# Optimization experiments

Hardware: AMD Instinct MI355X
Metric: run time of the kernel (lower is better)

Reference implementation:

```python
import jax, jax.numpy as jnp
import numpy as np

N = 100000   # nodes
E = 3200000  # edges
D = 256      # hidden_dim
G = 512      # graphs in batch
NEG_SLOPE = 0.2


def segment_softmax(logits, seg, num_segments):
    # numerically stable per-segment softmax over dim 0
    m = jax.ops.segment_max(logits, seg, num_segments=num_segments)
    m = jnp.where(jnp.isfinite(m), m, 0.0)  # empty segments -> 0
    e = jnp.exp(logits - m[seg])
    s = jax.ops.segment_sum(e, seg, num_segments=num_segments)
    return e / (s[seg] + 1e-16)


def setup_inputs() -> dict:
    key = jax.random.key(0)
    ks = jax.random.split(key, 6)
    x = jax.random.normal(ks[0], (N, D), dtype=jnp.float32)
    edge_index = jax.random.randint(ks[1], (2, E), 0, N, dtype=jnp.int32)
    batch = jnp.sort(jax.random.randint(ks[2], (N,), 0, G, dtype=jnp.int32))
    # GATConv(hidden_dim, 1) params (heads=1): lin weight, att vectors, bias
    W = jax.random.normal(ks[3], (D, 1), dtype=jnp.float32) / np.sqrt(D).astype(np.float32)
    att_src = jax.random.normal(ks[4], (1,), dtype=jnp.float32)
    att_dst = jax.random.normal(ks[5], (1,), dtype=jnp.float32)
    bias = jnp.zeros((1,), dtype=jnp.float32)
    return {"x": x, "edge_index": edge_index, "batch": batch,
            "W": W, "att_src": att_src, "att_dst": att_dst, "bias": bias}


def reference(x, edge_index, batch, W, att_src, att_dst, bias):
    n = x.shape[0]
    # --- GATConv(hidden_dim, 1), heads=1, add_self_loops=True ---
    h = x @ W                               # [N,1]
    a_s = (h * att_src).squeeze(-1)         # [N]
    a_d = (h * att_dst).squeeze(-1)         # [N]
    loops = jnp.arange(n, dtype=edge_index.dtype)
    src = jnp.concatenate([edge_index[0], loops])   # [E+N]
    dst = jnp.concatenate([edge_index[1], loops])   # [E+N]
    e = jax.nn.leaky_relu(a_s[src] + a_d[dst], NEG_SLOPE)
    alpha = segment_softmax(e, dst, n)               # softmax over incoming edges
    x_conv = jax.ops.segment_sum(alpha[:, None] * h[src], dst, num_segments=n) + bias  # [N,1]
    # --- segment softmax over graphs, then scatter-add pooling ---
    scores = segment_softmax(x_conv.squeeze(-1), batch, G)[:, None]  # [N,1]
    gx = jax.ops.segment_sum(x * scores, batch, num_segments=G)       # [G,D]
    return gx
```

## Files before the change

### kernel.cpp

```cpp
#include <hip/hip_runtime.h>
#include <stdint.h>

#define NEG_SLOPE 0.2f
#define DHID 256
#define BSZ_SHIFT 10
#define BSZ (1 << BSZ_SHIFT)
#define MAXNB 128
#define PSUB 16
#define SCHUNK 4096
#define KSUB 4

__device__ __forceinline__ float lrelu(float e) {
    return (e >= 0.0f) ? e : NEG_SLOPE * e;
}
__device__ __forceinline__ float dot4(float4 a, float4 b) {
    return a.x * b.x + a.y * b.y + a.z * b.z + a.w * b.w;
}

__global__ __launch_bounds__(256) void k1_h_bounds(
    const float* __restrict__ x, const float* __restrict__ W,
    float* __restrict__ h, int N,
    const int* __restrict__ batch, int* __restrict__ start, int G,
    float* __restrict__ gsum, int* __restrict__ cursor, int NB,
    int nRowBlk, int nBndBlk)
{
    if (blockIdx.x >= (unsigned)nRowBlk) {
        int rb = blockIdx.x - nRowBlk;
        if (rb == nBndBlk) {
            for (int t = threadIdx.x; t < G; t += 256) gsum[t] = 0.0f;
            for (int t = threadIdx.x; t < NB; t += 256) cursor[t] = 0;
            return;
        }
        int i = rb * 256 + threadIdx.x;
        if (i >= N) return;
        int b = batch[i];
        if (i == 0) {
            for (int g = 0; g <= b; ++g) start[g] = 0;
        } else {
            int bp = batch[i - 1];
            for (int g = bp + 1; g <= b; ++g) start[g] = i;
        }
        if (i == N - 1) {
            for (int g = b + 1; g <= G; ++g) start[g] = N;
        }
        return;
    }

    int wave = threadIdx.x >> 6;
    int lane = threadIdx.x & 63;
    int r = lane >> 4;
    int c = lane & 15;
    int row = blockIdx.x * 16 + wave * 4 + r;
    if (row >= N) return;

    float4 wv0 = *(const float4*)(W + c * 4);
    float4 wv1 = *(const float4*)(W + 64 + c * 4);
    float4 wv2 = *(const float4*)(W + 128 + c * 4);
    float4 wv3 = *(const float4*)(W + 192 + c * 4);
    const float* xr = x + (size_t)row * DHID;
    float4 a0 = *(const float4*)(xr + c * 4);
    float4 a1 = *(const float4*)(xr + 64 + c * 4);
    float4 a2 = *(const float4*)(xr + 128 + c * 4);
    float4 a3 = *(const float4*)(xr + 192 + c * 4);
    float s = dot4(a0, wv0) + dot4(a1, wv1) + dot4(a2, wv2) + dot4(a3, wv3);
    s += __shfl_xor(s, 1);
    s += __shfl_xor(s, 2);
    s += __shfl_xor(s, 4);
    s += __shfl_xor(s, 8);
    if (c == 0) h[row] = s;
}

__global__ __launch_bounds__(512) void k_scatter(
    const int* __restrict__ src, const int* __restrict__ dst, int E, int NB,
    int* __restrict__ cursor, uint32_t* __restrict__ pairs, int CAP)
{
    __shared__ int cnt[MAXNB];
    __shared__ int loff[MAXNB];
    __shared__ int base_g[MAXNB];
    __shared__ int lcur[MAXNB];
    __shared__ uint32_t buf[SCHUNK];
    __shared__ uint8_t binOf[SCHUNK];

    int e0 = blockIdx.x * SCHUNK;
    int e1 = min(e0 + SCHUNK, E);
    int nch = e1 - e0;
    int t = threadIdx.x;

    int sv[8], dv[8];
#pragma unroll
    for (int k = 0; k < 8; ++k) {
        int e = e0 + k * 512 + t;
        if (e < e1) { sv[k] = src[e]; dv[k] = dst[e]; }
    }

    for (int q = t; q < MAXNB; q += 512) { cnt[q] = 0; lcur[q] = 0; }
    __syncthreads();
#pragma unroll
    for (int k = 0; k < 8; ++k) {
        int e = e0 + k * 512 + t;
        if (e < e1) atomicAdd(&cnt[dv[k] >> BSZ_SHIFT], 1);
    }
    __syncthreads();
    if (t < 64) {
        int v0 = cnt[t], v1 = cnt[64 + t];
        int s0 = v0, s1 = v1;
#pragma unroll
        for (int d = 1; d < 64; d <<= 1) {
            int u0 = __shfl_up(s0, d);
            int u1 = __shfl_up(s1, d);
            if (t >= d) { s0 += u0; s1 += u1; }
        }
        int tot0 = __shfl(s0, 63);
        loff[t]      = s0 - v0;
        loff[64 + t] = s1 + tot0 - v1;
    }
    __syncthreads();
    for (int q = t; q < MAXNB; q += 512)
        if (q < NB && cnt[q] > 0) base_g[q] = atomicAdd(&cursor[q], cnt[q]);
    __syncthreads();
#pragma unroll
    for (int k = 0; k < 8; ++k) {
        int e = e0 + k * 512 + t;
        if (e < e1) {
            int d = dv[k];
            int bin = d >> BSZ_SHIFT;
            int r = atomicAdd(&lcur[bin], 1);
            int q = loff[bin] + r;
            buf[q] = ((uint32_t)sv[k] << BSZ_SHIFT) | (uint32_t)(d & (BSZ - 1));
            binOf[q] = (uint8_t)bin;
        }
    }
    __syncthreads();
    for (int q = t; q < nch; q += 512) {
        int b = binOf[q];
        pairs[(size_t)b * CAP + base_g[b] + (q - loff[b])] = buf[q];
    }
}

__global__ __launch_bounds__(256) void k_accum(
    const uint32_t* __restrict__ pairs, const int* __restrict__ cursor,
    const float* __restrict__ h,
    const float* __restrict__ att_src, const float* __restrict__ att_dst,
    float* __restrict__ partials, int N, int CAP)
{
    __shared__ float dacc[BSZ];
    __shared__ float nacc[BSZ];
    __shared__ float hbuf[BSZ];
    int b = blockIdx.x / PSUB;
    int s = blockIdx.x % PSUB;
    int base = b << BSZ_SHIFT;

    for (int t = threadIdx.x; t < BSZ; t += 256) {
        dacc[t] = 0.0f; nacc[t] = 0.0f;
        int gi = base + t;
        hbuf[t] = (gi < N) ? h[gi] : 0.0f;
    }
    __syncthreads();

    int count = cursor[b];
    int per = (count + PSUB - 1) / PSUB;
    int i0 = s * per;
    int i1 = min(i0 + per, count);

    float as = att_src[0], ad = att_dst[0];
    const uint32_t* bp = pairs + (size_t)b * CAP;
    for (int i = i0 + threadIdx.x; i < i1; i += 256) {
        uint32_t pr = bp[i];
        int ld = (int)(pr & (BSZ - 1));
        float hs = h[pr >> BSZ_SHIFT];
        float w = __expf(lrelu(as * hs + ad * hbuf[ld]));
        atomicAdd(&dacc[ld], w);
        atomicAdd(&nacc[ld], w * hs);
    }
    __syncthreads();
    float* out = partials + ((size_t)blockIdx.x * 2) * BSZ;
    for (int t = threadIdx.x; t < BSZ; t += 256) {
        out[t]       = dacc[t];
        out[BSZ + t] = nacc[t];
    }
}

__global__ __launch_bounds__(256) void k3_scores_p(
    const float* __restrict__ partials, const float* __restrict__ h,
    const float* __restrict__ att_src, const float* __restrict__ att_dst,
    const float* __restrict__ bias, const int* __restrict__ batch,
    float* __restrict__ escore, float* __restrict__ gsum, int N)
{
    __shared__ float bins[64];
    __shared__ int bbase_s;
    int i = blockIdx.x * 256 + threadIdx.x;
    if (threadIdx.x == 0) {
        int i0 = blockIdx.x * 256;
        bbase_s = batch[i0 < N ? i0 : N - 1];
    }
    for (int t = threadIdx.x; t < 64; t += 256) bins[t] = 0.0f;

    float w = 0.0f;
    int b = -1;
    if (i < N) {
        int bk = i >> BSZ_SHIFT;
        int pos = i & (BSZ - 1);
        float dsum = 0.0f, nsum = 0.0f;
#pragma unroll
        for (int p = 0; p < PSUB; ++p) {
            const float* pp = partials + ((size_t)(bk * PSUB + p) * 2) * BSZ;
            dsum += pp[pos];
            nsum += pp[BSZ + pos];
        }
        float hi = h[i];
        float e0 = lrelu((att_src[0] + att_dst[0]) * hi);
        float ws = __expf(e0);
        dsum += ws;
        nsum += ws * hi;
        float xc = nsum / (dsum + 1e-16f) + bias[0];
        w = __expf(xc);
        escore[i] = w;
        b = batch[i];
    }
    __syncthreads();
    if (i < N) {
        int off = b - bbase_s;
        if (off >= 0 && off < 64) atomicAdd(&bins[off], w);
        else                      atomicAdd(&gsum[b], w);
    }
    __syncthreads();
    for (int t = threadIdx.x; t < 64; t += 256)
        if (bins[t] != 0.0f) atomicAdd(&gsum[bbase_s + t], bins[t]);
}

__global__ __launch_bounds__(256) void k4_pool(
    const float* __restrict__ x, const float* __restrict__ escore,
    const float* __restrict__ gsum, const int* __restrict__ start,
    float* __restrict__ gxp, int G)
{
    int g = blockIdx.x >> 2;
    int s = blockIdx.x & 3;
    int st = start[g], en = start[g + 1];
    float inv = 1.0f / (gsum[g] + 1e-16f);
    int tid    = threadIdx.x;
    int col4   = (tid & 63) << 2;
    int rowOff = tid >> 6;

    float4 acc = make_float4(0.f, 0.f, 0.f, 0.f);
    int i = st + s * 4 + rowOff;
    for (; i + 16 < en; i += 32) {
        float sc0 = escore[i] * inv;
        float sc1 = escore[i + 16] * inv;
        float4 v0 = *(const float4*)(x + (size_t)i * DHID + col4);
        float4 v1 = *(const float4*)(x + (size_t)(i + 16) * DHID + col4);
        acc.x += v0.x * sc0 + v1.x * sc1;
        acc.y += v0.y * sc0 + v1.y * sc1;
        acc.z += v0.z * sc0 + v1.z * sc1;
        acc.w += v0.w * sc0 + v1.w * sc1;
    }
    if (i < en) {
        float sc = escore[i] * inv;
        float4 v = *(const float4*)(x + (size_t)i * DHID + col4);
        acc.x += v.x * sc; acc.y += v.y * sc;
        acc.z += v.z * sc; acc.w += v.w * sc;
    }

    __shared__ float4 red[256];
    red[tid] = acc;
    __syncthreads();
    if (tid < 64) {
        float4 a = red[tid], b = red[tid + 64], c = red[tid + 128], d = red[tid + 192];
        float4 r;
        r.x = a.x + b.x + c.x + d.x;
        r.y = a.y + b.y + c.y + d.y;
        r.z = a.z + b.z + c.z + d.z;
        r.w = a.w + b.w + c.w + d.w;
        *(float4*)(gxp + ((size_t)s * G + g) * DHID + col4) = r;
    }
}

__global__ __launch_bounds__(256) void k5_merge(
    const float* __restrict__ gxp, float* __restrict__ gx, int total)
{
    int j = blockIdx.x * 256 + threadIdx.x;
    if (j < total)
        gx[j] = gxp[j] + gxp[total + j] + gxp[2 * total + j] + gxp[3 * total + j];
}

__global__ __launch_bounds__(256) void k0_zero_fb(float* __restrict__ p, int n) {
    int i = blockIdx.x * 256 + threadIdx.x;
    if (i < n) p[i] = 0.0f;
}
__global__ __launch_bounds__(256) void k2_edges_fb(
    const int* __restrict__ src, const int* __restrict__ dst,
    const float* __restrict__ h,
    const float* __restrict__ att_src, const float* __restrict__ att_dst,
    float* __restrict__ denom, float* __restrict__ num, int E)
{
    int i = blockIdx.x * 256 + threadIdx.x;
    if (i >= E) return;
    int s = src[i], d = dst[i];
    float as = att_src[0], ad = att_dst[0];
    float hs = h[s];
    float w = expf(lrelu(as * hs + ad * h[d]));
    atomicAdd(&denom[d], w);
    atomicAdd(&num[d],   w * hs);
}
__global__ __launch_bounds__(256) void k3_scores_fb(
    const float* __restrict__ denom, const float* __restrict__ num,
    const float* __restrict__ h,
    const float* __restrict__ att_src, const float* __restrict__ att_dst,
    const float* __restrict__ bias, const int* __restrict__ batch,
    float* __restrict__ escore, float* __restrict__ gsum, int N)
{
    __shared__ float bins[64];
    __shared__ int bbase_s;
    int i = blockIdx.x * 256 + threadIdx.x;
    if (threadIdx.x == 0) {
        int i0 = blockIdx.x * 256;
        bbase_s = batch[i0 < N ? i0 : N - 1];
    }
    for (int t = threadIdx.x; t < 64; t += 256) bins[t] = 0.0f;
    float w = 0.0f;
    int b = -1;
    if (i < N) {
        float hi = h[i];
        float ws = expf(lrelu((att_src[0] + att_dst[0]) * hi));
        float dsum = denom[i] + ws;
        float nsum = num[i] + ws * hi;
        float xc = nsum / (dsum + 1e-16f) + bias[0];
        w = expf(xc);
        escore[i] = w;
        b = batch[i];
    }
    __syncthreads();
    if (i < N) {
        int off = b - bbase_s;
        if (off >= 0 && off < 64) atomicAdd(&bins[off], w);
        else                      atomicAdd(&gsum[b], w);
    }
    __syncthreads();
    for (int t = threadIdx.x; t < 64; t += 256)
        if (bins[t] != 0.0f) atomicAdd(&gsum[bbase_s + t], bins[t]);
}

extern "C" void kernel_launch(void* const* d_in, const int* in_sizes, int n_in,
                              void* d_out, int out_size, void* d_ws, size_t ws_size,
                              hipStream_t stream) {
    const float* x        = (const float*)d_in[0];
    const int*   eidx     = (const int*)d_in[1];
    const int*   batch    = (const int*)d_in[2];
    const float* W        = (const float*)d_in[3];
    const float* att_src  = (const float*)d_in[4];
    const float* att_dst  = (const float*)d_in[5];
    const float* bias     = (const float*)d_in[6];
    float*       gx       = (float*)d_out;

    const int N = in_sizes[2];
    const int E = in_sizes[1] / 2;
    const int G = out_size / DHID;
    const int NB = (N + BSZ - 1) >> BSZ_SHIFT;
    const int CAP = ((E / NB + 8192) + 255) & ~255;

    const int* src = eidx;
    const int* dst = eidx + E;

    char* p = (char*)d_ws;
    auto alloc = [&](size_t bytes) {
        char* q = p;
        p += (bytes + 255) & ~(size_t)255;
        return q;
    };
    float* h      = (float*)alloc((size_t)N * 4);
    float* escore = (float*)alloc((size_t)N * 4);
    float* gsum   = (float*)alloc((size_t)G * 4);
    int*   startA = (int*)alloc((size_t)(G + 1) * 4);

    size_t fixed = (size_t)(p - (char*)d_ws);
    size_t need_full = fixed
        + 512 + (size_t)NB * 4
        + 512 + (size_t)NB * CAP * 4
        + 512 + (size_t)NB * PSUB * 2 * BSZ * 4
        + 512 + (size_t)KSUB * G * DHID * 4;

    bool full = (NB <= MAXNB) && (N <= (1 << (32 - BSZ_SHIFT)))
             && (need_full + 4096 <= ws_size);

    int nRowBlk = (N + 15) / 16;
    int nBndBlk = (N + 255) / 256;

    if (full) {
        int*      cursor   = (int*)alloc((size_t)NB * 4);
        uint32_t* pairs    = (uint32_t*)alloc((size_t)NB * CAP * 4);
        float*    partials = (float*)alloc((size_t)NB * PSUB * 2 * BSZ * 4);
        float*    gxp      = (float*)alloc((size_t)KSUB * G * DHID * 4);

        int sgrid = (E + SCHUNK - 1) / SCHUNK;

        k1_h_bounds<<<nRowBlk + nBndBlk + 1, 256, 0, stream>>>(
            x, W, h, N, batch, startA, G, gsum, cursor, NB, nRowBlk, nBndBlk);
        k_scatter<<<sgrid, 512, 0, stream>>>(src, dst, E, NB, cursor,
                                             pairs, CAP);
        k_accum<<<NB * PSUB, 256, 0, stream>>>(pairs, cursor, h,
                                               att_src, att_dst, partials,
                                               N, CAP);
        k3_scores_p<<<(N + 255) / 256, 256, 0, stream>>>(partials, h,
                                                         att_src, att_dst, bias,
                                                         batch, escore, gsum, N);
        k4_pool<<<G * KSUB, 256, 0, stream>>>(x, escore, gsum, startA, gxp, G);
        k5_merge<<<(G * DHID + 255) / 256, 256, 0, stream>>>(gxp, gx, G * DHID);
    } else {
        float* denom = (float*)alloc((size_t)N * 4);
        float* num   = (float*)alloc((size_t)N * 4);
        float* gxp   = (float*)alloc((size_t)KSUB * G * DHID * 4);
        int*   dummyCur = (int*)alloc(256);
        k0_zero_fb<<<(2 * N + 255) / 256, 256, 0, stream>>>(denom, 2 * N);
        k1_h_bounds<<<nRowBlk + nBndBlk + 1, 256, 0, stream>>>(
            x, W, h, N, batch, startA, G, gsum, dummyCur, 0, nRowBlk, nBndBlk);
        k2_edges_fb<<<(E + 255) / 256, 256, 0, stream>>>(src, dst, h,
                                                         att_src, att_dst,
                                                         denom, num, E);
        k3_scores_fb<<<(N + 255) / 256, 256, 0, stream>>>(denom, num, h,
                                                          att_src, att_dst, bias,
                                                          batch, escore, gsum, N);
        k4_pool<<<G * KSUB, 256, 0, stream>>>(x, escore, gsum, startA, gxp, G);
        k5_merge<<<(G * DHID + 255) / 256, 256, 0, stream>>>(gxp, gx, G * DHID);
    }
}
```

Baseline: 109.8 us.

## Fuse edge scatter with h computation and bounds into one launch

Merges the edge-binning scatter kernel with the h = x@W matvec and graph-boundary kernels into a single 512-thread launch whose blocks are dispatched by block index. Cursor and gsum zeroing move to hipMemsetAsync calls. The scatter now reuses the rank returned by the counting atomic instead of a second atomic pass. The pooling loop is unrolled to four rows per iteration. This removes one kernel launch and the independent matvec can overlap the scatter. The cost is two extra memset operations and a larger shared-memory footprint on the matvec blocks.

```diff
diff --git a/kernel.cpp b/kernel.cpp
--- a/kernel.cpp
+++ b/kernel.cpp
@@ -17,21 +17,108 @@
     return a.x * b.x + a.y * b.y + a.z * b.z + a.w * b.w;
 }
 
-__global__ __launch_bounds__(256) void k1_h_bounds(
+__global__ __launch_bounds__(512) void kM1(
     const float* __restrict__ x, const float* __restrict__ W,
     float* __restrict__ h, int N,
     const int* __restrict__ batch, int* __restrict__ start, int G,
-    float* __restrict__ gsum, int* __restrict__ cursor, int NB,
-    int nRowBlk, int nBndBlk)
-{
-    if (blockIdx.x >= (unsigned)nRowBlk) {
-        int rb = blockIdx.x - nRowBlk;
-        if (rb == nBndBlk) {
-            for (int t = threadIdx.x; t < G; t += 256) gsum[t] = 0.0f;
-            for (int t = threadIdx.x; t < NB; t += 256) cursor[t] = 0;
-            return;
-        }
-        int i = rb * 256 + threadIdx.x;
+    const int* __restrict__ src, const int* __restrict__ dst, int E, int NB,
+    int* __restrict__ cursor, uint32_t* __restrict__ pairs, int CAP,
+    int nScat, int nRowBlk)
+{
+    __shared__ int cnt[MAXNB];
+    __shared__ int loff[MAXNB];
+    __shared__ int base_g[MAXNB];
+    __shared__ uint32_t buf[SCHUNK];
+    __shared__ uint8_t binOf[SCHUNK];
+
+    int bid = blockIdx.x;
+    int t = threadIdx.x;
+
+    if (bid < nScat) {
+        int e0 = bid * SCHUNK;
+        int e1 = min(e0 + SCHUNK, E);
+        int nch = e1 - e0;
+
+        int sv[8], dv[8], rk[8];
+#pragma unroll
+        for (int k = 0; k < 8; ++k) {
+            int e = e0 + k * 512 + t;
+            if (e < e1) { sv[k] = src[e]; dv[k] = dst[e]; }
+        }
+        for (int q = t; q < MAXNB; q += 512) cnt[q] = 0;
+        __syncthreads();
+#pragma unroll
+        for (int k = 0; k < 8; ++k) {
+            int e = e0 + k * 512 + t;
+            if (e < e1) rk[k] = atomicAdd(&cnt[dv[k] >> BSZ_SHIFT], 1);
+        }
+        __syncthreads();
+        if (t < 64) {
+            int v0 = cnt[t], v1 = cnt[64 + t];
+            int s0 = v0, s1 = v1;
+#pragma unroll
+            for (int d = 1; d < 64; d <<= 1) {
+                int u0 = __shfl_up(s0, d);
+                int u1 = __shfl_up(s1, d);
+                if (t >= d) { s0 += u0; s1 += u1; }
+            }
+            int tot0 = __shfl(s0, 63);
+            loff[t]      = s0 - v0;
+            loff[64 + t] = s1 + tot0 - v1;
+        }
+        __syncthreads();
+        for (int q = t; q < MAXNB; q += 512)
+            if (q < NB && cnt[q] > 0) base_g[q] = atomicAdd(&cursor[q], cnt[q]);
+        __syncthreads();
+#pragma unroll
+        for (int k = 0; k < 8; ++k) {
+            int e = e0 + k * 512 + t;
+            if (e < e1) {
+                int bin = dv[k] >> BSZ_SHIFT;
+                int q = loff[bin] + rk[k];
+                buf[q] = ((uint32_t)sv[k] << BSZ_SHIFT) |
+                         (uint32_t)(dv[k] & (BSZ - 1));
+                binOf[q] = (uint8_t)bin;
+            }
+        }
+        __syncthreads();
+        for (int q = t; q < nch; q += 512) {
+            int b = binOf[q];
+            pairs[(size_t)b * CAP + base_g[b] + (q - loff[b])] = buf[q];
+        }
+        return;
+    }
+
+    if (bid < nScat + nRowBlk) {
+        int rb = bid - nScat;
+        int wave = t >> 6;
+        int lane = t & 63;
+        int r = lane >> 4;
+        int c = lane & 15;
+        int row = rb * 32 + wave * 4 + r;
+        if (row >= N) return;
+
+        float4 wv0 = *(const float4*)(W + c * 4);
+        float4 wv1 = *(const float4*)(W + 64 + c * 4);
+        float4 wv2 = *(const float4*)(W + 128 + c * 4);
+        float4 wv3 = *(const float4*)(W + 192 + c * 4);
+        const float* xr = x + (size_t)row * DHID;
+        float4 a0 = *(const float4*)(xr + c * 4);
+        float4 a1 = *(const float4*)(xr + 64 + c * 4);
+        float4 a2 = *(const float4*)(xr + 128 + c * 4);
+        float4 a3 = *(const float4*)(xr + 192 + c * 4);
+        float s = dot4(a0, wv0) + dot4(a1, wv1) + dot4(a2, wv2) + dot4(a3, wv3);
+        s += __shfl_xor(s, 1);
+        s += __shfl_xor(s, 2);
+        s += __shfl_xor(s, 4);
+        s += __shfl_xor(s, 8);
+        if (c == 0) h[row] = s;
+        return;
+    }
+
+    {
+        int rb = bid - nScat - nRowBlk;
+        int i = rb * 512 + t;
         if (i >= N) return;
         int b = batch[i];
         if (i == 0) {
@@ -43,97 +130,6 @@
         if (i == N - 1) {
             for (int g = b + 1; g <= G; ++g) start[g] = N;
         }
-        return;
-    }
-
-    int wave = threadIdx.x >> 6;
-    int lane = threadIdx.x & 63;
-    int r = lane >> 4;
-    int c = lane & 15;
-    int row = blockIdx.x * 16 + wave * 4 + r;
-    if (row >= N) return;
-
-    float4 wv0 = *(const float4*)(W + c * 4);
-    float4 wv1 = *(const float4*)(W + 64 + c * 4);
-    float4 wv2 = *(const float4*)(W + 128 + c * 4);
-    float4 wv3 = *(const float4*)(W + 192 + c * 4);
-    const float* xr = x + (size_t)row * DHID;
-    float4 a0 = *(const float4*)(xr + c * 4);
-    float4 a1 = *(const float4*)(xr + 64 + c * 4);
-    float4 a2 = *(const float4*)(xr + 128 + c * 4);
-    float4 a3 = *(const float4*)(xr + 192 + c * 4);
-    float s = dot4(a0, wv0) + dot4(a1, wv1) + dot4(a2, wv2) + dot4(a3, wv3);
-    s += __shfl_xor(s, 1);
-    s += __shfl_xor(s, 2);
-    s += __shfl_xor(s, 4);
-    s += __shfl_xor(s, 8);
-    if (c == 0) h[row] = s;
-}
-
-__global__ __launch_bounds__(512) void k_scatter(
-    const int* __restrict__ src, const int* __restrict__ dst, int E, int NB,
-    int* __restrict__ cursor, uint32_t* __restrict__ pairs, int CAP)
-{
-    __shared__ int cnt[MAXNB];
-    __shared__ int loff[MAXNB];
-    __shared__ int base_g[MAXNB];
-    __shared__ int lcur[MAXNB];
-    __shared__ uint32_t buf[SCHUNK];
-    __shared__ uint8_t binOf[SCHUNK];
-
-    int e0 = blockIdx.x * SCHUNK;
-    int e1 = min(e0 + SCHUNK, E);
-    int nch = e1 - e0;
-    int t = threadIdx.x;
-
-    int sv[8], dv[8];
-#pragma unroll
-    for (int k = 0; k < 8; ++k) {
-        int e = e0 + k * 512 + t;
-        if (e < e1) { sv[k] = src[e]; dv[k] = dst[e]; }
-    }
-
-    for (int q = t; q < MAXNB; q += 512) { cnt[q] = 0; lcur[q] = 0; }
-    __syncthreads();
-#pragma unroll
-    for (int k = 0; k < 8; ++k) {
-        int e = e0 + k * 512 + t;
-        if (e < e1) atomicAdd(&cnt[dv[k] >> BSZ_SHIFT], 1);
-    }
-    __syncthreads();
-    if (t < 64) {
-        int v0 = cnt[t], v1 = cnt[64 + t];
-        int s0 = v0, s1 = v1;
-#pragma unroll
-        for (int d = 1; d < 64; d <<= 1) {
-            int u0 = __shfl_up(s0, d);
-            int u1 = __shfl_up(s1, d);
-            if (t >= d) { s0 += u0; s1 += u1; }
-        }
-        int tot0 = __shfl(s0, 63);
-        loff[t]      = s0 - v0;
-        loff[64 + t] = s1 + tot0 - v1;
-    }
-    __syncthreads();
-    for (int q = t; q < MAXNB; q += 512)
-        if (q < NB && cnt[q] > 0) base_g[q] = atomicAdd(&cursor[q], cnt[q]);
-    __syncthreads();
-#pragma unroll
-    for (int k = 0; k < 8; ++k) {
-        int e = e0 + k * 512 + t;
-        if (e < e1) {
-            int d = dv[k];
-            int bin = d >> BSZ_SHIFT;
-            int r = atomicAdd(&lcur[bin], 1);
-            int q = loff[bin] + r;
-            buf[q] = ((uint32_t)sv[k] << BSZ_SHIFT) | (uint32_t)(d & (BSZ - 1));
-            binOf[q] = (uint8_t)bin;
-        }
-    }
-    __syncthreads();
-    for (int q = t; q < nch; q += 512) {
-        int b = binOf[q];
-        pairs[(size_t)b * CAP + base_g[b] + (q - loff[b])] = buf[q];
     }
 }
 
@@ -243,17 +239,21 @@
 
     float4 acc = make_float4(0.f, 0.f, 0.f, 0.f);
     int i = st + s * 4 + rowOff;
-    for (; i + 16 < en; i += 32) {
+    for (; i + 48 < en; i += 64) {
         float sc0 = escore[i] * inv;
         float sc1 = escore[i + 16] * inv;
+        float sc2 = escore[i + 32] * inv;
+        float sc3 = escore[i + 48] * inv;
         float4 v0 = *(const float4*)(x + (size_t)i * DHID + col4);
         float4 v1 = *(const float4*)(x + (size_t)(i + 16) * DHID + col4);
-        acc.x += v0.x * sc0 + v1.x * sc1;
-        acc.y += v0.y * sc0 + v1.y * sc1;
-        acc.z += v0.z * sc0 + v1.z * sc1;
-        acc.w += v0.w * sc0 + v1.w * sc1;
-    }
-    if (i < en) {
+        float4 v2 = *(const float4*)(x + (size_t)(i + 32) * DHID + col4);
+        float4 v3 = *(const float4*)(x + (size_t)(i + 48) * DHID + col4);
+        acc.x += v0.x * sc0 + v1.x * sc1 + v2.x * sc2 + v3.x * sc3;
+        acc.y += v0.y * sc0 + v1.y * sc1 + v2.y * sc2 + v3.y * sc3;
+        acc.z += v0.z * sc0 + v1.z * sc1 + v2.z * sc2 + v3.z * sc3;
+        acc.w += v0.w * sc0 + v1.w * sc1 + v2.w * sc2 + v3.w * sc3;
+    }
+    for (; i < en; i += 16) {
         float sc = escore[i] * inv;
         float4 v = *(const float4*)(x + (size_t)i * DHID + col4);
         acc.x += v.x * sc; acc.y += v.y * sc;
@@ -381,8 +381,8 @@
     bool full = (NB <= MAXNB) && (N <= (1 << (32 - BSZ_SHIFT)))
              && (need_full + 4096 <= ws_size);
 
-    int nRowBlk = (N + 15) / 16;
-    int nBndBlk = (N + 255) / 256;
+    int nRowBlk = (N + 31) / 32;
+    int nBndBlk = (N + 511) / 512;
 
     if (full) {
         int*      cursor   = (int*)alloc((size_t)NB * 4);
@@ -390,12 +390,14 @@
         float*    partials = (float*)alloc((size_t)NB * PSUB * 2 * BSZ * 4);
         float*    gxp      = (float*)alloc((size_t)KSUB * G * DHID * 4);
 
-        int sgrid = (E + SCHUNK - 1) / SCHUNK;
-
-        k1_h_bounds<<<nRowBlk + nBndBlk + 1, 256, 0, stream>>>(
-            x, W, h, N, batch, startA, G, gsum, cursor, NB, nRowBlk, nBndBlk);
-        k_scatter<<<sgrid, 512, 0, stream>>>(src, dst, E, NB, cursor,
-                                             pairs, CAP);
+        int nScat = (E + SCHUNK - 1) / SCHUNK;
+
+        hipMemsetAsync(cursor, 0, (size_t)NB * 4, stream);
+        hipMemsetAsync(gsum, 0, (size_t)G * 4, stream);
+
+        kM1<<<nScat + nRowBlk + nBndBlk, 512, 0, stream>>>(
+            x, W, h, N, batch, startA, G,
+            src, dst, E, NB, cursor, pairs, CAP, nScat, nRowBlk);
         k_accum<<<NB * PSUB, 256, 0, stream>>>(pairs, cursor, h,
                                                att_src, att_dst, partials,
                                                N, CAP);
@@ -409,9 +411,11 @@
         float* num   = (float*)alloc((size_t)N * 4);
         float* gxp   = (float*)alloc((size_t)KSUB * G * DHID * 4);
         int*   dummyCur = (int*)alloc(256);
+        hipMemsetAsync(gsum, 0, (size_t)G * 4, stream);
         k0_zero_fb<<<(2 * N + 255) / 256, 256, 0, stream>>>(denom, 2 * N);
-        k1_h_bounds<<<nRowBlk + nBndBlk + 1, 256, 0, stream>>>(
-            x, W, h, N, batch, startA, G, gsum, dummyCur, 0, nRowBlk, nBndBlk);
+        kM1<<<nRowBlk + nBndBlk, 512, 0, stream>>>(
+            x, W, h, N, batch, startA, G,
+            src, dst, 0, 0, dummyCur, (uint32_t*)dummyCur, CAP, 0, nRowBlk);
         k2_edges_fb<<<(E + 255) / 256, 256, 0, stream>>>(src, dst, h,
                                                          att_src, att_dst,
                                                          denom, num, E);
```

After: 114.3 us. 4.0% more time.
